# Kernel tuning notes

Hardware: AMD Instinct MI355X
Metric: run time of the kernel (lower is better)

Reference implementation:

```python
import jax, jax.numpy as jnp
import numpy as np

N = 8192        # n_nodes
NFEAT = 512
NHID = 256
AVG_DEG = 32
K = 64          # mean_kwargs k
TEMP = 1.0      # mean_kwargs temperature


def setup_inputs() -> dict:
    key = jax.random.key(0)
    ks = jax.random.split(key, 5)
    x = jax.random.normal(ks[0], (N, NFEAT), jnp.float32)
    edge_index = jax.random.randint(ks[1], (2, N * AVG_DEG), 0, N, dtype=jnp.int64)
    W1 = jax.random.normal(ks[2], (NFEAT, NHID), jnp.float32) / np.sqrt(NFEAT)
    b1 = jnp.zeros((NHID,), jnp.float32)
    W2 = jax.random.normal(ks[3], (NHID, NHID), jnp.float32) / np.sqrt(NHID)
    b2 = jnp.zeros((NHID,), jnp.float32)
    return {"x": x, "edge_index": edge_index, "W1": W1, "b1": b1, "W2": W2, "b2": b2}


def _gcn_norm(edge_index, n, dtype):
    # PyG gcn_norm: add self-loops (weight 1), deg over col, sym normalization
    loops = jnp.arange(n, dtype=edge_index.dtype)
    row = jnp.concatenate([edge_index[0], loops])
    col = jnp.concatenate([edge_index[1], loops])
    w = jnp.ones(row.shape[0], dtype)
    deg = jnp.zeros((n,), dtype).at[col].add(w)
    dis = jnp.where(deg > 0, jax.lax.rsqrt(jnp.where(deg > 0, deg, 1.0)), 0.0)
    return row, col, dis[row] * w * dis[col]


def _soft_k_medoid(row, col, w, x):
    # soft_weighted_medoid_k_neighborhood(A, x, k=K, temperature=TEMP, with_weight_correction=True)
    n, d = x.shape
    A = jnp.zeros((n, n), x.dtype).at[row, col].add(w)   # coalesced dense adjacency
    topk_a, topk_idx = jax.lax.top_k(A, K)               # [n, K] neighbor weights / ids
    xk = x[topk_idx]                                     # [n, K, d]
    sq = jnp.sum(xk * xk, axis=-1)                       # [n, K]
    G = jnp.einsum('nkd,nld->nkl', xk, xk)               # Gram per node
    d2 = jnp.maximum(sq[:, :, None] + sq[:, None, :] - 2.0 * G, 0.0)
    pos = d2 > 0
    dist = jnp.where(pos, jnp.sqrt(jnp.where(pos, d2, 1.0)), 0.0)  # safe sqrt (grad-safe)
    # weighted sum of distances to each top-k candidate j: c[n,j] = sum_l a[n,l] * ||x_l - x_j||
    c = jnp.einsum('nl,nlj->nj', topk_a, dist)
    c = jnp.where(topk_a == 0, jnp.finfo(x.dtype).max, c)
    soft = jax.nn.softmax(-c / TEMP, axis=-1)            # [n, K]
    soft = soft * topk_a                                 # with_weight_correction
    soft = soft / jnp.sum(soft, axis=-1, keepdims=True)
    row_sum = jnp.sum(A, axis=-1)                        # preserve neighborhood mass
    return row_sum[:, None] * jnp.einsum('nk,nkd->nd', soft, xk)


def reference(x, edge_index, W1, b1, W2, b2):
    n = x.shape[0]
    row, col, w = _gcn_norm(edge_index, n, x.dtype)
    h = jax.nn.relu(_soft_k_medoid(row, col, w, x @ W1) + b1)   # gc1 + relu (dropout: eval = identity)
    return jax.nn.relu(_soft_k_medoid(row, col, w, h @ W2) + b2)  # gc2 + relu
```

## Files before the change

### kernel.cpp

```cpp
#include <hip/hip_runtime.h>

typedef _Float16 half4 __attribute__((ext_vector_type(4)));
typedef _Float16 half8 __attribute__((ext_vector_type(8)));
typedef float f32x4 __attribute__((ext_vector_type(4)));

#define NNODE 8192
#define NHID  256
#define RCAP  128
#define KCAP  64
#define GLS   72
#define SK    136

struct SmemGemm  { _Float16 sA[64][GLS]; _Float16 sB[64][GLS]; };
struct SmemDedup { int lc[2][RCAP]; float lw[2][RCAP]; unsigned char kp[2][RCAP];
                   int cw[2][2]; float rw[2][2]; };
struct SmemMedoid {
    _Float16 sh[64][SK];
    float s_a[64]; float s_sq[64]; float s_cpart[2][64]; float s_u[64];
    int s_cols[64]; float s_red[4][288]; float s_rsum;
};

__device__ __forceinline__ void gemm_body(
    char* smraw, const _Float16* __restrict__ Ahi, const _Float16* __restrict__ BT,
    _Float16* __restrict__ Chi, int K, int bm, int bn) {
    SmemGemm& sm = *(SmemGemm*)smraw;
    const int t = threadIdx.x;
    const int lane = t & 63, L15 = lane & 15, q = lane >> 4;
    const int w = t >> 6, wr = w >> 1, wc = w & 1;
    f32x4 acc[2][2];
#pragma unroll
    for (int a = 0; a < 2; ++a)
#pragma unroll
        for (int b2 = 0; b2 < 2; ++b2) acc[a][b2] = (f32x4){0.f, 0.f, 0.f, 0.f};

    for (int k0 = 0; k0 < K; k0 += 64) {
#pragma unroll
        for (int i = 0; i < 2; ++i) {
            int row = i * 32 + (t >> 3), ch = t & 7;
            *(half8*)&sm.sA[row][ch * 8] =
                *(const half8*)(Ahi + (size_t)(bm + row) * K + k0 + ch * 8);
            *(half8*)&sm.sB[row][ch * 8] =
                *(const half8*)(BT + (size_t)(bn + row) * K + k0 + ch * 8);
        }
        __syncthreads();
#pragma unroll
        for (int ks = 0; ks < 2; ++ks) {
            const int ko = ks * 32 + q * 8;
            half8 ah[2], bh[2];
#pragma unroll
            for (int tr = 0; tr < 2; ++tr)
                ah[tr] = *(const half8*)&sm.sA[32 * wr + 16 * tr + L15][ko];
#pragma unroll
            for (int tc = 0; tc < 2; ++tc)
                bh[tc] = *(const half8*)&sm.sB[32 * wc + 16 * tc + L15][ko];
#pragma unroll
            for (int tr = 0; tr < 2; ++tr)
#pragma unroll
                for (int tc = 0; tc < 2; ++tc)
                    acc[tr][tc] = __builtin_amdgcn_mfma_f32_16x16x32_f16(ah[tr], bh[tc], acc[tr][tc], 0, 0, 0);
        }
        __syncthreads();
    }
#pragma unroll
    for (int tr = 0; tr < 2; ++tr)
#pragma unroll
        for (int tc = 0; tc < 2; ++tc)
#pragma unroll
            for (int r = 0; r < 4; ++r) {
                int rowg = bm + 32 * wr + 16 * tr + q * 4 + r;
                int colg = bn + 32 * wc + 16 * tc + L15;
                Chi[(size_t)rowg * NHID + colg] = (_Float16)acc[tr][tc][r];
            }
}

__device__ __forceinline__ void dedup_body(
    char* smraw, const int* __restrict__ nbr, const int* __restrict__ rowcnt,
    const int* __restrict__ deg, int* __restrict__ cols, float* __restrict__ wout,
    float* __restrict__ rsum, int grp) {
    SmemDedup& sm = *(SmemDedup*)smraw;
    const int t = threadIdx.x;
    const int half = t >> 7, st = t & 127;
    const int wid = st >> 6, lane = t & 63;
    const int r = grp * 2 + half;
    int n = rowcnt[r]; if (n > RCAP) n = RCAP;
    if (st < n) sm.lc[half][st] = nbr[r * RCAP + st];
    __syncthreads();
    float dr = 1.f / sqrtf((float)deg[r]);
    bool keep = false; float wv = 0.f;
    if (st < n) {
        int c = sm.lc[half][st];
        int mult = 0; bool first = true;
        for (int i = 0; i < n; ++i) {
            int ci = sm.lc[half][i];
            if (ci == c) { mult++; if (i < st) first = false; }
        }
        keep = first;
        if (first) wv = (float)mult * dr * (1.f / sqrtf((float)deg[c]));
    }
    sm.kp[half][st] = keep ? 1 : 0; sm.lw[half][st] = wv;
    float rv = wv;
#pragma unroll
    for (int d = 1; d < 64; d <<= 1) rv += __shfl_xor(rv, d, 64);
    unsigned long long b = __ballot(keep);
    int pre = __popcll(b & ((1ull << lane) - 1ull));
    int cw = __popcll(b);
    if (lane == 0) { sm.cw[half][wid] = cw; sm.rw[half][wid] = rv; }
    __syncthreads();
    int total = sm.cw[half][0] + sm.cw[half][1];
    if (st == 0) rsum[r] = sm.rw[half][0] + sm.rw[half][1];
    const int base = r * KCAP;
    if (total <= KCAP) {
        int off = (wid ? sm.cw[half][0] : 0) + pre;
        if (keep) { cols[base + off] = sm.lc[half][st]; wout[base + off] = wv; }
        for (int m = total + st; m < KCAP; m += 128) { cols[base + m] = r; wout[base + m] = 0.f; }
    } else if (st == 0) {
        for (int s = 0; s < KCAP; ++s) {
            int best = -1;
            for (int i = 0; i < n; ++i) {
                if (!sm.kp[half][i]) continue;
                if (best < 0 || sm.lw[half][i] > sm.lw[half][best] ||
                    (sm.lw[half][i] == sm.lw[half][best] && sm.lc[half][i] < sm.lc[half][best])) best = i;
            }
            cols[base + s] = sm.lc[half][best]; wout[base + s] = sm.lw[half][best]; sm.kp[half][best] = 0;
        }
    }
}

__device__ __forceinline__ void medoid_core(
    SmemMedoid& sm, const _Float16* __restrict__ Xhi, const float* __restrict__ bias,
    float* __restrict__ OutF, _Float16* __restrict__ OutHi, int node, int writeH) {
    const int t = threadIdx.x;
    const int w = t >> 6, lane = t & 63;
    const int L15 = lane & 15, q = lane >> 4;
    const int wr = w >> 1, wc = w & 1;

    f32x4 acc[2][2];
#pragma unroll
    for (int a = 0; a < 2; ++a)
#pragma unroll
        for (int b = 0; b < 2; ++b) acc[a][b] = (f32x4){0.f, 0.f, 0.f, 0.f};

    const int ch = t & 15, rr = t >> 4;
    for (int phase = 0; phase < 2; ++phase) {
#pragma unroll
        for (int i = 0; i < 4; ++i) {
            int l = i * 16 + rr;
            *(half8*)&sm.sh[l][ch * 8] =
                *(const half8*)(Xhi + ((size_t)sm.s_cols[l] << 8) + phase * 128 + ch * 8);
        }
        __syncthreads();
#pragma unroll
        for (int ks = 0; ks < 4; ++ks) {
            const int ko = ks * 32 + q * 8;
            half8 ah[2], bh[2];
#pragma unroll
            for (int tr = 0; tr < 2; ++tr) ah[tr] = *(const half8*)&sm.sh[32 * wr + 16 * tr + L15][ko];
#pragma unroll
            for (int tc = 0; tc < 2; ++tc) bh[tc] = *(const half8*)&sm.sh[32 * wc + 16 * tc + L15][ko];
#pragma unroll
            for (int tr = 0; tr < 2; ++tr)
#pragma unroll
                for (int tc = 0; tc < 2; ++tc)
                    acc[tr][tc] = __builtin_amdgcn_mfma_f32_16x16x32_f16(ah[tr], bh[tc], acc[tr][tc], 0, 0, 0);
        }
        if (phase == 0) __syncthreads();
    }

#pragma unroll
    for (int tr = 0; tr < 2; ++tr)
#pragma unroll
        for (int tc = 0; tc < 2; ++tc)
            if (32 * wr + 16 * tr == 32 * wc + 16 * tc) {
#pragma unroll
                for (int r = 0; r < 4; ++r)
                    if (L15 == q * 4 + r) sm.s_sq[32 * wr + 16 * tr + L15] = acc[tr][tc][r];
            }
    __syncthreads();

    f32x4 sq4[2], a4[2];
#pragma unroll
    for (int tr = 0; tr < 2; ++tr) {
        sq4[tr] = *(const f32x4*)&sm.s_sq[32 * wr + 16 * tr + 4 * q];
        a4[tr]  = *(const f32x4*)&sm.s_a [32 * wr + 16 * tr + 4 * q];
    }
#pragma unroll
    for (int tc = 0; tc < 2; ++tc) {
        const int colg = 32 * wc + 16 * tc + L15;
        const float sqc = sm.s_sq[colg];
        float pj = 0.f;
#pragma unroll
        for (int tr = 0; tr < 2; ++tr)
#pragma unroll
            for (int r = 0; r < 4; ++r) {
                float d2 = sq4[tr][r] + sqc - 2.f * acc[tr][tc][r];
                float dist = d2 > 0.f ? __builtin_amdgcn_sqrtf(d2) : 0.f;
                pj = fmaf(a4[tr][r], dist, pj);
            }
        pj += __shfl_xor(pj, 16, 64);
        pj += __shfl_xor(pj, 32, 64);
        if (q == 0) sm.s_cpart[wr][colg] = pj;
    }
    __syncthreads();

    if (w == 0) {
        int j = lane;
        float c = sm.s_cpart[0][j] + sm.s_cpart[1][j];
        float aj = sm.s_a[j];
        bool valid = aj > 0.f;
        float cv = valid ? c : 3.4e38f;
        float mn = cv;
#pragma unroll
        for (int d = 1; d < 64; d <<= 1) mn = fminf(mn, __shfl_xor(mn, d, 64));
        float e = valid ? __expf(mn - c) * aj : 0.f;
        float s = e;
#pragma unroll
        for (int d = 1; d < 64; d <<= 1) s += __shfl_xor(s, d, 64);
        sm.s_u[j] = e * (sm.s_rsum / s);
    }
    __syncthreads();

    const int oct = t & 31, jb = t >> 5;
    float accd[8] = {0.f, 0.f, 0.f, 0.f, 0.f, 0.f, 0.f, 0.f};
#pragma unroll
    for (int jj = 0; jj < 8; ++jj) {
        int j = jb * 8 + jj;
        float u = sm.s_u[j];
        half8 xv;
        if (oct < 16) xv = *(const half8*)(Xhi + ((size_t)sm.s_cols[j] << 8) + oct * 8);
        else          xv = *(const half8*)&sm.sh[j][(oct - 16) * 8];
#pragma unroll
        for (int e = 0; e < 8; ++e) accd[e] = fmaf(u, (float)xv[e], accd[e]);
    }
#pragma unroll
    for (int e = 0; e < 8; ++e) accd[e] += __shfl_xor(accd[e], 32, 64);
    if (lane < 32) {
#pragma unroll
        for (int e = 0; e < 8; ++e) sm.s_red[w][9 * oct + e] = accd[e];
    }
    __syncthreads();
    const int idx = 9 * (t >> 3) + (t & 7);
    float o = sm.s_red[0][idx] + sm.s_red[1][idx] + sm.s_red[2][idx] + sm.s_red[3][idx];
    float res = fmaxf(o + bias[t], 0.f);
    size_t oi = (size_t)node * NHID + t;
    if (writeH) OutHi[oi] = (_Float16)res;
    else        OutF[oi] = res;
}

#define PREPB 512
__global__ __launch_bounds__(256) void k_prep_scatter(
    const float* __restrict__ x, _Float16* __restrict__ xh,
    const float* __restrict__ W1, _Float16* __restrict__ w1T,
    const float* __restrict__ W2, _Float16* __restrict__ w2T,
    const void* edges, int* rowcnt, int* nbr, int* deg, int E) {
    const int t = threadIdx.x;
    if ((int)blockIdx.x < PREPB) {
        const int gid = blockIdx.x * 256 + t, nthr = PREPB * 256;
        for (int i = gid; i < NNODE * 512 / 4; i += nthr) {
            float4 v = ((const float4*)x)[i];
            half4 h;
            h[0] = (_Float16)v.x; h[1] = (_Float16)v.y;
            h[2] = (_Float16)v.z; h[3] = (_Float16)v.w;
            *(half4*)&xh[4 * (size_t)i] = h;
        }
        for (int i = gid; i < 512 * NHID; i += nthr) {
            int k = i >> 8, n = i & 255;
            w1T[(size_t)n * 512 + k] = (_Float16)W1[i];
        }
        for (int i = gid; i < NHID * NHID; i += nthr) {
            int k = i >> 8, n = i & 255;
            w2T[(size_t)n * 256 + k] = (_Float16)W2[i];
        }
    } else {
        __shared__ int sflag;
        if (t < 64) {
            const long long* e = (const long long*)edges;
            long long v = e[t];
            unsigned long long bad = __ballot(v < 0 || v >= (long long)NNODE);
            if (t == 0) sflag = (bad == 0) ? 1 : 0;
        }
        __syncthreads();
        const int fl = sflag;
        int i = ((int)blockIdx.x - PREPB) * 256 + t;
        if (i >= E + NNODE) return;
        int r, c;
        if (i < E) {
            if (fl) {
                const long long* e = (const long long*)edges;
                r = (int)e[i]; c = (int)e[E + i];
            } else {
                const int* e = (const int*)edges;
                r = e[i]; c = e[E + i];
            }
        } else { r = i - E; c = r; }
        int pos = atomicAdd(&rowcnt[r], 1);
        if (pos < RCAP) nbr[r * RCAP + pos] = c;
        atomicAdd(&deg[c], 1);
    }
}

__global__ __launch_bounds__(256) void k_gemm1_dedup(
    const _Float16* __restrict__ xh, const _Float16* __restrict__ w1T,
    _Float16* __restrict__ X1,
    const int* __restrict__ nbr, const int* __restrict__ rowcnt,
    const int* __restrict__ deg,
    int* __restrict__ cols, float* __restrict__ wA, float* __restrict__ rsum) {
    __shared__ __align__(16) char smem[sizeof(SmemGemm)];
    if ((int)blockIdx.x < 512) {
        int g = blockIdx.x;
        gemm_body(smem, xh, w1T, X1, 512, (g >> 2) * 64, (g & 3) * 64);
    } else {
        dedup_body(smem, nbr, rowcnt, deg, cols, wA, rsum, (int)blockIdx.x - 512);
    }
}

__global__ __launch_bounds__(256, 6) void k_medoid(
    const _Float16* __restrict__ X, const float* __restrict__ bias,
    float* __restrict__ OutF, _Float16* __restrict__ OutHi,
    const int* __restrict__ cols, const float* __restrict__ wts,
    const float* __restrict__ rsum, int writeH) {
    __shared__ __align__(16) SmemMedoid sm;
    const int node = blockIdx.x, t = threadIdx.x;
    if (t < 64) { sm.s_cols[t] = cols[node * KCAP + t]; sm.s_a[t] = wts[node * KCAP + t]; }
    if (t == 0) sm.s_rsum = rsum[node];
    __syncthreads();
    medoid_core(sm, X, bias, OutF, OutHi, node, writeH);
}

__global__ __launch_bounds__(256) void k_gemm2(
    const _Float16* __restrict__ Hh, const _Float16* __restrict__ w2T,
    _Float16* __restrict__ X2) {
    __shared__ __align__(16) char smem[sizeof(SmemGemm)];
    gemm_body(smem, Hh, w2T, X2, 256, blockIdx.x * 64, blockIdx.y * 64);
}

extern "C" void kernel_launch(void* const* d_in, const int* in_sizes, int n_in,
                              void* d_out, int out_size, void* d_ws, size_t ws_size,
                              hipStream_t stream) {
    const float* x  = (const float*)d_in[0];
    const void*  ei = d_in[1];
    const float* W1 = (const float*)d_in[2];
    const float* b1 = (const float*)d_in[3];
    const float* W2 = (const float*)d_in[4];
    const float* b2 = (const float*)d_in[5];
    float* out = (float*)d_out;
    const int E = in_sizes[1] / 2;

    char* p = (char*)d_ws;
    auto alloc = [&](size_t bytes) { char* q = p; p += (bytes + 255) & ~(size_t)255; return q; };
    int*      cnt    = (int*)alloc((size_t)2 * NNODE * 4);
    int*      deg    = cnt;
    int*      rowcnt = cnt + NNODE;
    int*      colsA  = (int*)alloc((size_t)NNODE * KCAP * 4);
    float*    wAr    = (float*)alloc((size_t)NNODE * KCAP * 4);
    float*    rsum   = (float*)alloc((size_t)NNODE * 4);
    _Float16* xh     = (_Float16*)alloc((size_t)NNODE * 512 * 2);
    _Float16* w1T    = (_Float16*)alloc((size_t)512 * NHID * 2);
    _Float16* w2T    = (_Float16*)alloc((size_t)NHID * NHID * 2);
    _Float16* X1     = (_Float16*)alloc((size_t)NNODE * NHID * 2);
    _Float16* Hh     = (_Float16*)alloc((size_t)NNODE * NHID * 2);
    int*      nbr    = (int*)alloc((size_t)NNODE * RCAP * 4);

    const int nscat = (E + NNODE + 255) / 256;

    hipMemsetAsync(cnt, 0, (size_t)2 * NNODE * 4, stream);
    k_prep_scatter<<<PREPB + nscat, 256, 0, stream>>>(x, xh, W1, w1T, W2, w2T,
                                                      ei, rowcnt, nbr, deg, E);
    k_gemm1_dedup<<<512 + NNODE / 2, 256, 0, stream>>>(xh, w1T, X1, nbr, rowcnt, deg,
                                                       colsA, wAr, rsum);
    k_medoid<<<NNODE, 256, 0, stream>>>(X1, b1, nullptr, Hh, colsA, wAr, rsum, 1);
    k_gemm2<<<dim3(NNODE / 64, NHID / 64), 256, 0, stream>>>(Hh, w2T, X1);
    k_medoid<<<NNODE, 256, 0, stream>>>(X1, b2, out, nullptr, colsA, wAr, rsum, 0);
}
```

Before: 212.4 us.

## Prefetch second gather half during MFMA and alias reduction buffer onto tile smem

The medoid kernel now issues the global gather of the second 128-column half into registers before running the MFMAs on the first half, so gather latency overlaps with compute. The reduction buffer s_red is placed in a union with the gathered tile to cut shared memory per block, a barrier is added before it is overwritten, and launch bounds rise to 8 blocks per SM for more occupancy. The extra live registers for the prefetch and the tighter register budget from the higher occupancy target could cause spills.

```diff
diff --git a/kernel.cpp b/kernel.cpp
--- a/kernel.cpp
+++ b/kernel.cpp
@@ -15,9 +15,12 @@
 struct SmemDedup { int lc[2][RCAP]; float lw[2][RCAP]; unsigned char kp[2][RCAP];
                    int cw[2][2]; float rw[2][2]; };
 struct SmemMedoid {
-    _Float16 sh[64][SK];
+    union {
+        _Float16 sh[64][SK];
+        float s_red[4][288];
+    };
     float s_a[64]; float s_sq[64]; float s_cpart[2][64]; float s_u[64];
-    int s_cols[64]; float s_red[4][288]; float s_rsum;
+    int s_cols[64]; float s_rsum;
 };
 
 __device__ __forceinline__ void gemm_body(
@@ -141,29 +144,54 @@
         for (int b = 0; b < 2; ++b) acc[a][b] = (f32x4){0.f, 0.f, 0.f, 0.f};
 
     const int ch = t & 15, rr = t >> 4;
-    for (int phase = 0; phase < 2; ++phase) {
-#pragma unroll
-        for (int i = 0; i < 4; ++i) {
-            int l = i * 16 + rr;
-            *(half8*)&sm.sh[l][ch * 8] =
-                *(const half8*)(Xhi + ((size_t)sm.s_cols[l] << 8) + phase * 128 + ch * 8);
-        }
-        __syncthreads();
-#pragma unroll
-        for (int ks = 0; ks < 4; ++ks) {
-            const int ko = ks * 32 + q * 8;
-            half8 ah[2], bh[2];
-#pragma unroll
-            for (int tr = 0; tr < 2; ++tr) ah[tr] = *(const half8*)&sm.sh[32 * wr + 16 * tr + L15][ko];
-#pragma unroll
-            for (int tc = 0; tc < 2; ++tc) bh[tc] = *(const half8*)&sm.sh[32 * wc + 16 * tc + L15][ko];
-#pragma unroll
-            for (int tr = 0; tr < 2; ++tr)
-#pragma unroll
-                for (int tc = 0; tc < 2; ++tc)
-                    acc[tr][tc] = __builtin_amdgcn_mfma_f32_16x16x32_f16(ah[tr], bh[tc], acc[tr][tc], 0, 0, 0);
-        }
-        if (phase == 0) __syncthreads();
+    const _Float16* rbase[4];
+#pragma unroll
+    for (int i = 0; i < 4; ++i)
+        rbase[i] = Xhi + ((size_t)sm.s_cols[i * 16 + rr] << 8) + ch * 8;
+
+    half8 g0[4];
+#pragma unroll
+    for (int i = 0; i < 4; ++i) g0[i] = *(const half8*)rbase[i];
+#pragma unroll
+    for (int i = 0; i < 4; ++i) *(half8*)&sm.sh[i * 16 + rr][ch * 8] = g0[i];
+    __syncthreads();
+
+    half8 g1[4];
+#pragma unroll
+    for (int i = 0; i < 4; ++i) g1[i] = *(const half8*)(rbase[i] + 128);
+
+#pragma unroll
+    for (int ks = 0; ks < 4; ++ks) {
+        const int ko = ks * 32 + q * 8;
+        half8 ah[2], bh[2];
+#pragma unroll
+        for (int tr = 0; tr < 2; ++tr) ah[tr] = *(const half8*)&sm.sh[32 * wr + 16 * tr + L15][ko];
+#pragma unroll
+        for (int tc = 0; tc < 2; ++tc) bh[tc] = *(const half8*)&sm.sh[32 * wc + 16 * tc + L15][ko];
+#pragma unroll
+        for (int tr = 0; tr < 2; ++tr)
+#pragma unroll
+            for (int tc = 0; tc < 2; ++tc)
+                acc[tr][tc] = __builtin_amdgcn_mfma_f32_16x16x32_f16(ah[tr], bh[tc], acc[tr][tc], 0, 0, 0);
+    }
+    __syncthreads();
+
+#pragma unroll
+    for (int i = 0; i < 4; ++i) *(half8*)&sm.sh[i * 16 + rr][ch * 8] = g1[i];
+    __syncthreads();
+#pragma unroll
+    for (int ks = 0; ks < 4; ++ks) {
+        const int ko = ks * 32 + q * 8;
+        half8 ah[2], bh[2];
+#pragma unroll
+        for (int tr = 0; tr < 2; ++tr) ah[tr] = *(const half8*)&sm.sh[32 * wr + 16 * tr + L15][ko];
+#pragma unroll
+        for (int tc = 0; tc < 2; ++tc) bh[tc] = *(const half8*)&sm.sh[32 * wc + 16 * tc + L15][ko];
+#pragma unroll
+        for (int tr = 0; tr < 2; ++tr)
+#pragma unroll
+            for (int tc = 0; tc < 2; ++tc)
+                acc[tr][tc] = __builtin_amdgcn_mfma_f32_16x16x32_f16(ah[tr], bh[tc], acc[tr][tc], 0, 0, 0);
     }
 
 #pragma unroll
@@ -233,6 +261,7 @@
     }
 #pragma unroll
     for (int e = 0; e < 8; ++e) accd[e] += __shfl_xor(accd[e], 32, 64);
+    __syncthreads();
     if (lane < 32) {
 #pragma unroll
         for (int e = 0; e < 8; ++e) sm.s_red[w][9 * oct + e] = accd[e];
@@ -313,7 +342,7 @@
     }
 }
 
-__global__ __launch_bounds__(256, 6) void k_medoid(
+__global__ __launch_bounds__(256, 8) void k_medoid(
     const _Float16* __restrict__ X, const float* __restrict__ bias,
     float* __restrict__ OutF, _Float16* __restrict__ OutHi,
     const int* __restrict__ cols, const float* __restrict__ wts,
```

Result: faster. 196.6 us (-7.5%).

## Process one node per wavefront in medoid kernel using symmetric Gram tiles

Applied to the files above, without the earlier changes.

Rewrites the medoid kernel so each 64-lane wave handles a whole node, with four nodes per block. The Gram matrix is computed straight from global memory into registers, using only the 10 upper-triangular 16x16 MFMA tiles and exploiting symmetry for the column sums. This removes the shared-memory staging, the block-wide __syncthreads, and the cross-wave reductions. The costs are heavier register use (launch bounds lowered to 5), gathers from global memory without LDS reuse, and reliance on same-wave LDS ordering through wave barriers.

```diff
diff --git a/kernel.cpp b/kernel.cpp
--- a/kernel.cpp
+++ b/kernel.cpp
@@ -9,16 +9,11 @@
 #define RCAP  128
 #define KCAP  64
 #define GLS   72
-#define SK    136
 
 struct SmemGemm  { _Float16 sA[64][GLS]; _Float16 sB[64][GLS]; };
 struct SmemDedup { int lc[2][RCAP]; float lw[2][RCAP]; unsigned char kp[2][RCAP];
                    int cw[2][2]; float rw[2][2]; };
-struct SmemMedoid {
-    _Float16 sh[64][SK];
-    float s_a[64]; float s_sq[64]; float s_cpart[2][64]; float s_u[64];
-    int s_cols[64]; float s_red[4][288]; float s_rsum;
-};
+struct SmemMedoidW { float sq[64]; float cst[64]; float av[64]; };
 
 __device__ __forceinline__ void gemm_body(
     char* smraw, const _Float16* __restrict__ Ahi, const _Float16* __restrict__ BT,
@@ -126,124 +121,147 @@
     }
 }
 
-__device__ __forceinline__ void medoid_core(
-    SmemMedoid& sm, const _Float16* __restrict__ Xhi, const float* __restrict__ bias,
-    float* __restrict__ OutF, _Float16* __restrict__ OutHi, int node, int writeH) {
+#define TILE_OFF(r, c, A) { \
+    const float sqc = sm.sq[16*(c) + L15]; \
+    const float acl = sm.av[16*(c) + L15]; \
+    float pj = 0.f; float pt[4]; \
+    _Pragma("unroll") \
+    for (int i = 0; i < 4; ++i) { \
+        float d2 = sm.sq[16*(r) + q*4 + i] + sqc - 2.f * (A)[i]; \
+        float dist = d2 > 0.f ? __builtin_amdgcn_sqrtf(d2) : 0.f; \
+        pj = fmaf(sm.av[16*(r) + q*4 + i], dist, pj); \
+        pt[i] = acl * dist; \
+    } \
+    pj += __shfl_xor(pj, 16, 64); pj += __shfl_xor(pj, 32, 64); \
+    if (q == 0) sm.cst[16*(c) + L15] += pj; \
+    _Pragma("unroll") \
+    for (int i = 0; i < 4; ++i) { \
+        pt[i] += __shfl_xor(pt[i], 1, 64); \
+        pt[i] += __shfl_xor(pt[i], 2, 64); \
+        pt[i] += __shfl_xor(pt[i], 4, 64); \
+        pt[i] += __shfl_xor(pt[i], 8, 64); \
+    } \
+    if (L15 == 0) { \
+        sm.cst[16*(r) + q*4 + 0] += pt[0]; \
+        sm.cst[16*(r) + q*4 + 1] += pt[1]; \
+        sm.cst[16*(r) + q*4 + 2] += pt[2]; \
+        sm.cst[16*(r) + q*4 + 3] += pt[3]; \
+    } }
+
+#define TILE_DIAG(g, A) { \
+    const float sqc = sm.sq[16*(g) + L15]; \
+    float pj = 0.f; \
+    _Pragma("unroll") \
+    for (int i = 0; i < 4; ++i) { \
+        float d2 = sm.sq[16*(g) + q*4 + i] + sqc - 2.f * (A)[i]; \
+        float dist = d2 > 0.f ? __builtin_amdgcn_sqrtf(d2) : 0.f; \
+        pj = fmaf(sm.av[16*(g) + q*4 + i], dist, pj); \
+    } \
+    pj += __shfl_xor(pj, 16, 64); pj += __shfl_xor(pj, 32, 64); \
+    if (q == 0) sm.cst[16*(g) + L15] += pj; }
+
+#define MFMA16(a, b, c) __builtin_amdgcn_mfma_f32_16x16x32_f16((a), (b), (c), 0, 0, 0)
+
+__global__ __launch_bounds__(256, 5) void k_medoid(
+    const _Float16* __restrict__ X, const float* __restrict__ bias,
+    float* __restrict__ OutF, _Float16* __restrict__ OutHi,
+    const int* __restrict__ cols, const float* __restrict__ wts,
+    const float* __restrict__ rsum, int writeH) {
+    __shared__ SmemMedoidW smw[4];
     const int t = threadIdx.x;
     const int w = t >> 6, lane = t & 63;
+    const int node = (int)blockIdx.x * 4 + w;
+    SmemMedoidW& sm = smw[w];
     const int L15 = lane & 15, q = lane >> 4;
-    const int wr = w >> 1, wc = w & 1;
-
-    f32x4 acc[2][2];
-#pragma unroll
-    for (int a = 0; a < 2; ++a)
-#pragma unroll
-        for (int b = 0; b < 2; ++b) acc[a][b] = (f32x4){0.f, 0.f, 0.f, 0.f};
-
-    const int ch = t & 15, rr = t >> 4;
-    for (int phase = 0; phase < 2; ++phase) {
-#pragma unroll
-        for (int i = 0; i < 4; ++i) {
-            int l = i * 16 + rr;
-            *(half8*)&sm.sh[l][ch * 8] =
-                *(const half8*)(Xhi + ((size_t)sm.s_cols[l] << 8) + phase * 128 + ch * 8);
-        }
-        __syncthreads();
-#pragma unroll
-        for (int ks = 0; ks < 4; ++ks) {
-            const int ko = ks * 32 + q * 8;
-            half8 ah[2], bh[2];
-#pragma unroll
-            for (int tr = 0; tr < 2; ++tr) ah[tr] = *(const half8*)&sm.sh[32 * wr + 16 * tr + L15][ko];
-#pragma unroll
-            for (int tc = 0; tc < 2; ++tc) bh[tc] = *(const half8*)&sm.sh[32 * wc + 16 * tc + L15][ko];
-#pragma unroll
-            for (int tr = 0; tr < 2; ++tr)
-#pragma unroll
-                for (int tc = 0; tc < 2; ++tc)
-                    acc[tr][tc] = __builtin_amdgcn_mfma_f32_16x16x32_f16(ah[tr], bh[tc], acc[tr][tc], 0, 0, 0);
-        }
-        if (phase == 0) __syncthreads();
-    }
-
-#pragma unroll
-    for (int tr = 0; tr < 2; ++tr)
-#pragma unroll
-        for (int tc = 0; tc < 2; ++tc)
-            if (32 * wr + 16 * tr == 32 * wc + 16 * tc) {
-#pragma unroll
-                for (int r = 0; r < 4; ++r)
-                    if (L15 == q * 4 + r) sm.s_sq[32 * wr + 16 * tr + L15] = acc[tr][tc][r];
-            }
-    __syncthreads();
-
-    f32x4 sq4[2], a4[2];
-#pragma unroll
-    for (int tr = 0; tr < 2; ++tr) {
-        sq4[tr] = *(const f32x4*)&sm.s_sq[32 * wr + 16 * tr + 4 * q];
-        a4[tr]  = *(const f32x4*)&sm.s_a [32 * wr + 16 * tr + 4 * q];
-    }
-#pragma unroll
-    for (int tc = 0; tc < 2; ++tc) {
-        const int colg = 32 * wc + 16 * tc + L15;
-        const float sqc = sm.s_sq[colg];
-        float pj = 0.f;
-#pragma unroll
-        for (int tr = 0; tr < 2; ++tr)
-#pragma unroll
-            for (int r = 0; r < 4; ++r) {
-                float d2 = sq4[tr][r] + sqc - 2.f * acc[tr][tc][r];
-                float dist = d2 > 0.f ? __builtin_amdgcn_sqrtf(d2) : 0.f;
-                pj = fmaf(a4[tr][r], dist, pj);
-            }
-        pj += __shfl_xor(pj, 16, 64);
-        pj += __shfl_xor(pj, 32, 64);
-        if (q == 0) sm.s_cpart[wr][colg] = pj;
-    }
-    __syncthreads();
-
-    if (w == 0) {
-        int j = lane;
-        float c = sm.s_cpart[0][j] + sm.s_cpart[1][j];
-        float aj = sm.s_a[j];
-        bool valid = aj > 0.f;
-        float cv = valid ? c : 3.4e38f;
-        float mn = cv;
-#pragma unroll
-        for (int d = 1; d < 64; d <<= 1) mn = fminf(mn, __shfl_xor(mn, d, 64));
-        float e = valid ? __expf(mn - c) * aj : 0.f;
-        float s = e;
-#pragma unroll
-        for (int d = 1; d < 64; d <<= 1) s += __shfl_xor(s, d, 64);
-        sm.s_u[j] = e * (sm.s_rsum / s);
-    }
-    __syncthreads();
-
-    const int oct = t & 31, jb = t >> 5;
-    float accd[8] = {0.f, 0.f, 0.f, 0.f, 0.f, 0.f, 0.f, 0.f};
-#pragma unroll
-    for (int jj = 0; jj < 8; ++jj) {
-        int j = jb * 8 + jj;
-        float u = sm.s_u[j];
-        half8 xv;
-        if (oct < 16) xv = *(const half8*)(Xhi + ((size_t)sm.s_cols[j] << 8) + oct * 8);
-        else          xv = *(const half8*)&sm.sh[j][(oct - 16) * 8];
-#pragma unroll
-        for (int e = 0; e < 8; ++e) accd[e] = fmaf(u, (float)xv[e], accd[e]);
-    }
-#pragma unroll
-    for (int e = 0; e < 8; ++e) accd[e] += __shfl_xor(accd[e], 32, 64);
+
+    const int   base    = node * KCAP;
+    const int   cid_own = cols[base + lane];
+    const float a_own   = wts[base + lane];
+    const float rs      = rsum[node];
+
+    sm.av[lane]  = a_own;
+    sm.cst[lane] = 0.f;
+
+    const _Float16* rb[4];
+#pragma unroll
+    for (int g = 0; g < 4; ++g) {
+        int cg = __shfl(cid_own, g * 16 + L15, 64);
+        rb[g] = X + ((size_t)cg << 8) + q * 8;
+    }
+
+    f32x4 a00 = (f32x4){0.f,0.f,0.f,0.f}, a01 = a00, a02 = a00, a03 = a00;
+    f32x4 a11 = a00, a12 = a00, a13 = a00, a22 = a00, a23 = a00, a33 = a00;
+
+#pragma unroll
+    for (int kc = 0; kc < 8; ++kc) {
+        half8 f0 = *(const half8*)(rb[0] + kc * 32);
+        half8 f1 = *(const half8*)(rb[1] + kc * 32);
+        half8 f2 = *(const half8*)(rb[2] + kc * 32);
+        half8 f3 = *(const half8*)(rb[3] + kc * 32);
+        a00 = MFMA16(f0, f0, a00); a01 = MFMA16(f0, f1, a01);
+        a02 = MFMA16(f0, f2, a02); a03 = MFMA16(f0, f3, a03);
+        a11 = MFMA16(f1, f1, a11); a12 = MFMA16(f1, f2, a12);
+        a13 = MFMA16(f1, f3, a13); a22 = MFMA16(f2, f2, a22);
+        a23 = MFMA16(f2, f3, a23); a33 = MFMA16(f3, f3, a33);
+    }
+
+#pragma unroll
+    for (int i = 0; i < 4; ++i)
+        if (L15 == q * 4 + i) {
+            sm.sq[ 0 + L15] = a00[i];
+            sm.sq[16 + L15] = a11[i];
+            sm.sq[32 + L15] = a22[i];
+            sm.sq[48 + L15] = a33[i];
+        }
+    __builtin_amdgcn_wave_barrier();
+
+    TILE_DIAG(0, a00) TILE_DIAG(1, a11) TILE_DIAG(2, a22) TILE_DIAG(3, a33)
+    TILE_OFF(0, 1, a01) TILE_OFF(0, 2, a02) TILE_OFF(0, 3, a03)
+    TILE_OFF(1, 2, a12) TILE_OFF(1, 3, a13) TILE_OFF(2, 3, a23)
+
+    __builtin_amdgcn_wave_barrier();
+    const float cj = sm.cst[lane];
+    const bool valid = a_own > 0.f;
+    float mn = valid ? cj : 3.4e38f;
+#pragma unroll
+    for (int d = 1; d < 64; d <<= 1) mn = fminf(mn, __shfl_xor(mn, d, 64));
+    float e = valid ? __expf(mn - cj) * a_own : 0.f;
+    float s = e;
+#pragma unroll
+    for (int d = 1; d < 64; d <<= 1) s += __shfl_xor(s, d, 64);
+    const float u_own = e * (rs / s);
+
+    const int d8 = (lane & 31) * 8, jo = lane >> 5;
+    float o[8] = {0.f,0.f,0.f,0.f,0.f,0.f,0.f,0.f};
+#pragma unroll
+    for (int it = 0; it < 32; ++it) {
+        int j = it * 2 + jo;
+        float u  = __shfl(u_own, j, 64);
+        int  cj2 = __shfl(cid_own, j, 64);
+        half8 xv = *(const half8*)(X + ((size_t)cj2 << 8) + d8);
+#pragma unroll
+        for (int e2 = 0; e2 < 8; ++e2) o[e2] = fmaf(u, (float)xv[e2], o[e2]);
+    }
+#pragma unroll
+    for (int e2 = 0; e2 < 8; ++e2) o[e2] += __shfl_xor(o[e2], 32, 64);
     if (lane < 32) {
-#pragma unroll
-        for (int e = 0; e < 8; ++e) sm.s_red[w][9 * oct + e] = accd[e];
-    }
-    __syncthreads();
-    const int idx = 9 * (t >> 3) + (t & 7);
-    float o = sm.s_red[0][idx] + sm.s_red[1][idx] + sm.s_red[2][idx] + sm.s_red[3][idx];
-    float res = fmaxf(o + bias[t], 0.f);
-    size_t oi = (size_t)node * NHID + t;
-    if (writeH) OutHi[oi] = (_Float16)res;
-    else        OutF[oi] = res;
+        float4 ba = *(const float4*)&bias[d8];
+        float4 bb = *(const float4*)&bias[d8 + 4];
+        float r0 = fmaxf(o[0] + ba.x, 0.f), r1 = fmaxf(o[1] + ba.y, 0.f);
+        float r2 = fmaxf(o[2] + ba.z, 0.f), r3 = fmaxf(o[3] + ba.w, 0.f);
+        float r4 = fmaxf(o[4] + bb.x, 0.f), r5 = fmaxf(o[5] + bb.y, 0.f);
+        float r6 = fmaxf(o[6] + bb.z, 0.f), r7 = fmaxf(o[7] + bb.w, 0.f);
+        size_t ob = (size_t)node * NHID + d8;
+        if (writeH) {
+            half8 hv;
+            hv[0] = (_Float16)r0; hv[1] = (_Float16)r1; hv[2] = (_Float16)r2; hv[3] = (_Float16)r3;
+            hv[4] = (_Float16)r4; hv[5] = (_Float16)r5; hv[6] = (_Float16)r6; hv[7] = (_Float16)r7;
+            *(half8*)&OutHi[ob] = hv;
+        } else {
+            *(float4*)&OutF[ob]     = make_float4(r0, r1, r2, r3);
+            *(float4*)&OutF[ob + 4] = make_float4(r4, r5, r6, r7);
+        }
+    }
 }
 
 #define PREPB 512
@@ -313,19 +331,6 @@
     }
 }
 
-__global__ __launch_bounds__(256, 6) void k_medoid(
-    const _Float16* __restrict__ X, const float* __restrict__ bias,
-    float* __restrict__ OutF, _Float16* __restrict__ OutHi,
-    const int* __restrict__ cols, const float* __restrict__ wts,
-    const float* __restrict__ rsum, int writeH) {
-    __shared__ __align__(16) SmemMedoid sm;
-    const int node = blockIdx.x, t = threadIdx.x;
-    if (t < 64) { sm.s_cols[t] = cols[node * KCAP + t]; sm.s_a[t] = wts[node * KCAP + t]; }
-    if (t == 0) sm.s_rsum = rsum[node];
-    __syncthreads();
-    medoid_core(sm, X, bias, OutF, OutHi, node, writeH);
-}
-
 __global__ __launch_bounds__(256) void k_gemm2(
     const _Float16* __restrict__ Hh, const _Float16* __restrict__ w2T,
     _Float16* __restrict__ X2) {
@@ -367,7 +372,7 @@
                                                       ei, rowcnt, nbr, deg, E);
     k_gemm1_dedup<<<512 + NNODE / 2, 256, 0, stream>>>(xh, w1T, X1, nbr, rowcnt, deg,
                                                        colsA, wAr, rsum);
-    k_medoid<<<NNODE, 256, 0, stream>>>(X1, b1, nullptr, Hh, colsA, wAr, rsum, 1);
+    k_medoid<<<NNODE / 4, 256, 0, stream>>>(X1, b1, nullptr, Hh, colsA, wAr, rsum, 1);
     k_gemm2<<<dim3(NNODE / 64, NHID / 64), 256, 0, stream>>>(Hh, w2T, X1);
-    k_medoid<<<NNODE, 256, 0, stream>>>(X1, b2, out, nullptr, colsA, wAr, rsum, 0);
-}
+    k_medoid<<<NNODE / 4, 256, 0, stream>>>(X1, b2, out, nullptr, colsA, wAr, rsum, 0);
+}
```

Result: slower. 317.1 us (+49.3%).
